# Optimization experiments

Measured on AMD Instinct MI355X. Metric: run time of the kernel, lower is better.

The kernel has to match this reference:

```python
import jax, jax.numpy as jnp
import numpy as np

NEG = -1e30  # finite stand-in for -inf (keeps logaddexp grads NaN-free)

def setup_inputs() -> dict:
    key = jax.random.key(0)
    k1, k2, k3 = jax.random.split(key, 3)
    T, B, V, S = 512, 32, 4096, 64
    acts = jax.random.normal(k1, (T, B, V), dtype=jnp.float32)
    labels = jax.random.randint(k2, (B * S,), 1, V, dtype=jnp.int32)  # blank=0 excluded
    input_lengths = jax.random.randint(k3, (B,), T // 2, T + 1, dtype=jnp.int32)
    target_lengths = jnp.full((B,), S, dtype=jnp.int32)
    return {"acts": acts, "labels": labels, "input_lengths": input_lengths,
            "target_lengths": target_lengths}

def _ctc_cost(acts, labels, input_lengths, target_lengths):
    T, B, V = acts.shape
    S = labels.shape[0] // B
    L = 2 * S + 1  # extended label length (blanks interleaved)
    log_probs = jax.nn.log_softmax(acts, axis=-1)          # (T,B,V)
    lab = labels.reshape(B, S)
    ext = jnp.zeros((B, L), dtype=lab.dtype).at[:, 1::2].set(lab)  # blank,l1,blank,...
    # gather per-timestep log-probs of extended labels: (T,B,L)
    lp_ext = jnp.take_along_axis(log_probs, jnp.broadcast_to(ext[None], (T, B, L)), axis=2)
    # skip transition allowed when ext[s] is non-blank and differs from ext[s-2]
    ext_m2 = jnp.concatenate([jnp.zeros((B, 2), ext.dtype), ext[:, :-2]], axis=1)
    skip = (jnp.arange(L)[None, :] >= 2) & (ext != 0) & (ext != ext_m2)  # (B,L)
    alpha0 = jnp.full((B, L), NEG, dtype=log_probs.dtype)
    alpha0 = alpha0.at[:, 0].set(lp_ext[0, :, 0]).at[:, 1].set(lp_ext[0, :, 1])
    negcol = jnp.full((B, 1), NEG, dtype=log_probs.dtype)

    def step(alpha, xt):
        lp_t, t = xt
        a1 = jnp.concatenate([negcol, alpha[:, :-1]], axis=1)
        a2 = jnp.concatenate([negcol, negcol, alpha[:, :-2]], axis=1)
        a2 = jnp.where(skip, a2, NEG)
        new = jnp.logaddexp(jnp.logaddexp(alpha, a1), a2) + lp_t
        # freeze alpha once t >= input_length so the final row holds alpha at t=len-1
        alpha = jnp.where((t < input_lengths)[:, None], new, alpha)
        return alpha, None

    alpha_T, _ = jax.lax.scan(step, alpha0, (lp_ext[1:], jnp.arange(1, T)))
    idx_hi = (2 * target_lengths).astype(jnp.int32)        # last blank
    idx_lo = jnp.maximum(idx_hi - 1, 0)                    # last label
    a_hi = jnp.take_along_axis(alpha_T, idx_hi[:, None], axis=1)[:, 0]
    a_lo = jnp.take_along_axis(alpha_T, idx_lo[:, None], axis=1)[:, 0]
    nll = -jnp.logaddexp(a_hi, a_lo)                        # (B,)
    nll = jnp.where(jnp.isinf(nll) | (nll > 1e29), 0.0, nll)  # masked_fill(isinf, 0)
    return jnp.sum(nll)  # size_average=False, length_average=False

def reference(acts, labels, input_lengths, target_lengths):
    return _ctc_cost(acts, labels, input_lengths, target_lengths)
```

## Files before the change

### kernel.cpp

```cpp
#include <hip/hip_runtime.h>
#include <hip/hip_bf16.h>

constexpr int T = 512;
constexpr int B = 32;
constexpr int V = 4096;
constexpr int S = 64;
constexpr int GW = S + 1;

#define NEG (-1e30f)

__device__ inline float lae2(float a, float b) {
    float m = fmaxf(a, b);
    return m + __logf(__expf(a - m) + __expf(b - m));
}
__device__ inline float lae3(float a, float b, float c) {
    float m = fmaxf(fmaxf(a, b), c);
    return m + __logf(__expf(a - m) + __expf(b - m) + __expf(c - m));
}

__global__ __launch_bounds__(256) void lse_gather_kernel(
    const float* __restrict__ acts, const int* __restrict__ labels,
    float* __restrict__ g) {
    int tb = blockIdx.x;
    int t = tb >> 5;
    int b = tb & 31;
    const float* row = acts + (size_t)tb * V;
    int tid = threadIdx.x;

    float4 r[4];
    float vmax = -INFINITY;
#pragma unroll
    for (int j = 0; j < 4; ++j) {
        r[j] = reinterpret_cast<const float4*>(row)[j * 256 + tid];
        vmax = fmaxf(vmax, fmaxf(fmaxf(r[j].x, r[j].y), fmaxf(r[j].z, r[j].w)));
    }
#pragma unroll
    for (int off = 1; off < 64; off <<= 1)
        vmax = fmaxf(vmax, __shfl_xor(vmax, off));

    __shared__ float smax[4];
    __shared__ float ssum[4];
    int wid = tid >> 6;
    if ((tid & 63) == 0) smax[wid] = vmax;
    __syncthreads();
    vmax = fmaxf(fmaxf(smax[0], smax[1]), fmaxf(smax[2], smax[3]));

    float acc = 0.f;
#pragma unroll
    for (int j = 0; j < 4; ++j) {
        acc += __expf(r[j].x - vmax) + __expf(r[j].y - vmax) +
               __expf(r[j].z - vmax) + __expf(r[j].w - vmax);
    }
#pragma unroll
    for (int off = 1; off < 64; off <<= 1)
        acc += __shfl_xor(acc, off);
    if ((tid & 63) == 0) ssum[wid] = acc;
    __syncthreads();
    float lse = vmax + __logf(ssum[0] + ssum[1] + ssum[2] + ssum[3]);

    if (tid < GW) {
        int sym = (tid == 0) ? 0 : labels[b * S + tid - 1];
        g[((size_t)b * T + t) * GW + tid] = row[sym] - lse;
    }
}

__global__ __launch_bounds__(64) void ctc_fwd_kernel(
    const float* __restrict__ g, const int* __restrict__ labels,
    const int* __restrict__ in_len, const int* __restrict__ tgt_len,
    float* __restrict__ out) {
    int b = blockIdx.x;
    int lane = threadIdx.x;
    const float* gb = g + (size_t)b * T * GW;

    int myLab = labels[b * S + lane];
    bool skip1 = (lane >= 1) && (myLab != labels[b * S + lane - 1]);

    float lpb = gb[0];
    float lpl = gb[1 + lane];
    float a0 = (lane == 0) ? lpb : NEG;
    float a1 = (lane == 0) ? lpl : NEG;
    float a2 = NEG;

    int Tl = in_len[b];

    float nlpb = gb[GW];
    float nlpl = gb[GW + 1 + lane];

    for (int t = 1; t < Tl; ++t) {
        lpb = nlpb;
        lpl = nlpl;
        if (t + 1 < Tl) {
            nlpb = gb[(size_t)(t + 1) * GW];
            nlpl = gb[(size_t)(t + 1) * GW + 1 + lane];
        }
        float pa1 = __shfl_up(a1, 1);
        if (lane == 0) pa1 = NEG;

        float n0 = lae2(a0, pa1) + lpb;
        float n1 = lae3(a1, a0, skip1 ? pa1 : NEG) + lpl;
        float n2 = lae2(a2, a1) + lpb;
        a0 = n0; a1 = n1; a2 = n2;
    }

    int tl = tgt_len[b];
    float ahi, alo;
    if (tl >= S) {
        ahi = __shfl(a2, 63);
        alo = __shfl(a1, S - 1);
    } else if (tl >= 1) {
        ahi = __shfl(a0, tl);
        alo = __shfl(a1, tl - 1);
    } else {
        ahi = __shfl(a0, 0);
        alo = ahi;
    }

    if (lane == 0) {
        float m = fmaxf(ahi, alo);
        float nll = -(m + __logf(__expf(ahi - m) + __expf(alo - m)));
        if (!(nll < 1e29f)) nll = 0.f;
        atomicAdd(out, nll);
    }
}

extern "C" void kernel_launch(void* const* d_in, const int* in_sizes, int n_in,
                              void* d_out, int out_size, void* d_ws, size_t ws_size,
                              hipStream_t stream) {
    const float* acts = (const float*)d_in[0];
    const int* labels = (const int*)d_in[1];
    const int* in_len = (const int*)d_in[2];
    const int* tgt_len = (const int*)d_in[3];
    float* out = (float*)d_out;
    float* g = (float*)d_ws;

    hipMemsetAsync(out, 0, sizeof(float), stream);

    lse_gather_kernel<<<T * B, 256, 0, stream>>>(acts, labels, g);
    ctc_fwd_kernel<<<B, 64, 0, stream>>>(g, labels, in_len, tgt_len, out);
}
```

Measured before the change: 501.4 us.

## Use one wave per row in LSE gather and double-buffer the CTC recursion through LDS

```diff
diff --git a/kernel.cpp b/kernel.cpp
--- a/kernel.cpp
+++ b/kernel.cpp
@@ -5,7 +5,8 @@
 constexpr int B = 32;
 constexpr int V = 4096;
 constexpr int S = 64;
-constexpr int GW = S + 1;
+constexpr int GW2 = 68;
+constexpr int CH = 120;
 
 #define NEG (-1e30f)
 
@@ -21,105 +22,133 @@
 __global__ __launch_bounds__(256) void lse_gather_kernel(
     const float* __restrict__ acts, const int* __restrict__ labels,
     float* __restrict__ g) {
-    int tb = blockIdx.x;
-    int t = tb >> 5;
-    int b = tb & 31;
-    const float* row = acts + (size_t)tb * V;
-    int tid = threadIdx.x;
+    int w = blockIdx.x * 4 + (threadIdx.x >> 6);
+    int lane = threadIdx.x & 63;
+    int t = w >> 5;
+    int b = w & 31;
+    const float* row = acts + (size_t)w * V;
+    const float4* row4 = reinterpret_cast<const float4*>(row);
 
-    float4 r[4];
+    float4 r[16];
     float vmax = -INFINITY;
 #pragma unroll
-    for (int j = 0; j < 4; ++j) {
-        r[j] = reinterpret_cast<const float4*>(row)[j * 256 + tid];
+    for (int j = 0; j < 16; ++j) {
+        r[j] = row4[j * 64 + lane];
         vmax = fmaxf(vmax, fmaxf(fmaxf(r[j].x, r[j].y), fmaxf(r[j].z, r[j].w)));
     }
 #pragma unroll
     for (int off = 1; off < 64; off <<= 1)
         vmax = fmaxf(vmax, __shfl_xor(vmax, off));
 
-    __shared__ float smax[4];
-    __shared__ float ssum[4];
-    int wid = tid >> 6;
-    if ((tid & 63) == 0) smax[wid] = vmax;
-    __syncthreads();
-    vmax = fmaxf(fmaxf(smax[0], smax[1]), fmaxf(smax[2], smax[3]));
-
     float acc = 0.f;
 #pragma unroll
-    for (int j = 0; j < 4; ++j) {
+    for (int j = 0; j < 16; ++j) {
         acc += __expf(r[j].x - vmax) + __expf(r[j].y - vmax) +
                __expf(r[j].z - vmax) + __expf(r[j].w - vmax);
     }
 #pragma unroll
     for (int off = 1; off < 64; off <<= 1)
         acc += __shfl_xor(acc, off);
-    if ((tid & 63) == 0) ssum[wid] = acc;
-    __syncthreads();
-    float lse = vmax + __logf(ssum[0] + ssum[1] + ssum[2] + ssum[3]);
 
-    if (tid < GW) {
-        int sym = (tid == 0) ? 0 : labels[b * S + tid - 1];
-        g[((size_t)b * T + t) * GW + tid] = row[sym] - lse;
-    }
+    float lse = vmax + __logf(acc);
+
+    float* grow = g + (size_t)(b * T + t) * GW2;
+    int sym = labels[b * S + lane];
+    grow[1 + lane] = row[sym] - lse;
+    if (lane == 0) grow[0] = row[0] - lse;
 }
 
-__global__ __launch_bounds__(64) void ctc_fwd_kernel(
+__global__ __launch_bounds__(256) void ctc_fwd_kernel(
     const float* __restrict__ g, const int* __restrict__ labels,
     const int* __restrict__ in_len, const int* __restrict__ tgt_len,
     float* __restrict__ out) {
+    __shared__ float sg[2][CH][GW2];
     int b = blockIdx.x;
-    int lane = threadIdx.x;
-    const float* gb = g + (size_t)b * T * GW;
+    int tid = threadIdx.x;
+    int lane = tid & 63;
+    int wave = tid >> 6;
+    const float* gb = g + (size_t)b * T * GW2;
+    int Tl = in_len[b];
+    int nch = (Tl + CH - 1) / CH;
 
-    int myLab = labels[b * S + lane];
-    bool skip1 = (lane >= 1) && (myLab != labels[b * S + lane - 1]);
+    {
+        int tcnt = min(CH, Tl);
+        int F4 = tcnt * (GW2 / 4);
+        const float4* src = reinterpret_cast<const float4*>(gb);
+        float4* dst = reinterpret_cast<float4*>(&sg[0][0][0]);
+        for (int i = tid; i < F4; i += 256) dst[i] = src[i];
+    }
+    __syncthreads();
 
-    float lpb = gb[0];
-    float lpl = gb[1 + lane];
-    float a0 = (lane == 0) ? lpb : NEG;
-    float a1 = (lane == 0) ? lpl : NEG;
-    float a2 = NEG;
-
-    int Tl = in_len[b];
-
-    float nlpb = gb[GW];
-    float nlpl = gb[GW + 1 + lane];
-
-    for (int t = 1; t < Tl; ++t) {
-        lpb = nlpb;
-        lpl = nlpl;
-        if (t + 1 < Tl) {
-            nlpb = gb[(size_t)(t + 1) * GW];
-            nlpl = gb[(size_t)(t + 1) * GW + 1 + lane];
-        }
-        float pa1 = __shfl_up(a1, 1);
-        if (lane == 0) pa1 = NEG;
-
-        float n0 = lae2(a0, pa1) + lpb;
-        float n1 = lae3(a1, a0, skip1 ? pa1 : NEG) + lpl;
-        float n2 = lae2(a2, a1) + lpb;
-        a0 = n0; a1 = n1; a2 = n2;
+    float a0 = NEG, a1 = NEG, a2 = NEG;
+    bool skip1 = false;
+    if (wave == 0) {
+        int myLab = labels[b * S + lane];
+        skip1 = (lane >= 1) && (myLab != labels[b * S + lane - 1]);
+        float lpb0 = sg[0][0][0];
+        float lpl0 = sg[0][0][1 + lane];
+        a0 = (lane == 0) ? lpb0 : NEG;
+        a1 = (lane == 0) ? lpl0 : NEG;
     }
 
-    int tl = tgt_len[b];
-    float ahi, alo;
-    if (tl >= S) {
-        ahi = __shfl(a2, 63);
-        alo = __shfl(a1, S - 1);
-    } else if (tl >= 1) {
-        ahi = __shfl(a0, tl);
-        alo = __shfl(a1, tl - 1);
-    } else {
-        ahi = __shfl(a0, 0);
-        alo = ahi;
+    int t = 1;
+    for (int c = 0; c < nch; ++c) {
+        int buf = c & 1;
+        int tEnd = min((c + 1) * CH, Tl);
+        if (wave == 0) {
+            int tc = t - c * CH;
+            int tcEnd = tEnd - c * CH;
+            if (tc < tcEnd) {
+                float lpb = sg[buf][tc][0];
+                float lpl = sg[buf][tc][1 + lane];
+                for (; tc < tcEnd; ++tc) {
+                    float nlpb = 0.f, nlpl = 0.f;
+                    if (tc + 1 < tcEnd) {
+                        nlpb = sg[buf][tc + 1][0];
+                        nlpl = sg[buf][tc + 1][1 + lane];
+                    }
+                    float pa1 = __shfl_up(a1, 1);
+                    if (lane == 0) pa1 = NEG;
+                    float n0 = lae2(a0, pa1) + lpb;
+                    float n1 = lae3(a1, a0, skip1 ? pa1 : NEG) + lpl;
+                    float n2 = lae2(a2, a1) + lpb;
+                    a0 = n0; a1 = n1; a2 = n2;
+                    lpb = nlpb; lpl = nlpl;
+                }
+            }
+            t = tEnd;
+        } else {
+            int t0 = (c + 1) * CH;
+            if (t0 < Tl) {
+                int tcnt = min(CH, Tl - t0);
+                int F4 = tcnt * (GW2 / 4);
+                const float4* src = reinterpret_cast<const float4*>(gb + (size_t)t0 * GW2);
+                float4* dst = reinterpret_cast<float4*>(&sg[(c + 1) & 1][0][0]);
+                for (int i = tid - 64; i < F4; i += 192) dst[i] = src[i];
+            }
+        }
+        __syncthreads();
     }
 
-    if (lane == 0) {
-        float m = fmaxf(ahi, alo);
-        float nll = -(m + __logf(__expf(ahi - m) + __expf(alo - m)));
-        if (!(nll < 1e29f)) nll = 0.f;
-        atomicAdd(out, nll);
+    if (tid < 64) {
+        int tl = tgt_len[b];
+        float ahi, alo;
+        if (tl >= S) {
+            ahi = __shfl(a2, 63);
+            alo = __shfl(a1, S - 1);
+        } else if (tl >= 1) {
+            ahi = __shfl(a0, tl);
+            alo = __shfl(a1, tl - 1);
+        } else {
+            ahi = __shfl(a0, 0);
+            alo = ahi;
+        }
+        if (lane == 0) {
+            float m = fmaxf(ahi, alo);
+            float nll = -(m + __logf(__expf(ahi - m) + __expf(alo - m)));
+            if (!(nll < 1e29f)) nll = 0.f;
+            atomicAdd(out, nll);
+        }
     }
 }
 
@@ -135,6 +164,6 @@
 
     hipMemsetAsync(out, 0, sizeof(float), stream);
 
-    lse_gather_kernel<<<T * B, 256, 0, stream>>>(acts, labels, g);
-    ctc_fwd_kernel<<<B, 64, 0, stream>>>(g, labels, in_len, tgt_len, out);
+    lse_gather_kernel<<<(T * B) / 4, 256, 0, stream>>>(acts, labels, g);
+    ctc_fwd_kernel<<<B, 256, 0, stream>>>(g, labels, in_len, tgt_len, out);
 }
```

New measurement: 482.5 us. 3.8% less time.
